# Kernel tuning notes

Measured on AMD Instinct MI355X. Metric: run time of the kernel, lower is better.

## Reference

```python
import jax, jax.numpy as jnp
import numpy as np

B, T, N, H, E, R = 512, 10, 50, 200, 10000, 200

def _aggregate(neigh, neigh_len, hist_len, ids, rids, ent, rel, Wa, ba, v):
    # neigh: [B,T,N] entity ids; returns padded GRU input [B,T,3H]
    h = Wa.shape[0]
    e = ent[neigh]                                  # [B,T,N,h] neighbor embeds
    se = ent[ids]                                   # [B,h]
    re_a = ent[rids]                                # faithful: original uses ent_embeds[r] in attention
    Wn, Ws, Wr = Wa[:, :h], Wa[:, h:2 * h], Wa[:, 2 * h:]
    pre = jnp.einsum('btnh,gh->btng', e, Wn) + (se @ Ws.T + re_a @ Wr.T + ba)[:, None, None, :]
    logits = (jnp.tanh(pre) @ v)[..., 0]            # [B,T,N]
    nmask = jnp.arange(neigh.shape[2])[None, None, :] < neigh_len[:, :, None]
    logits = jnp.where(nmask, logits, -1e30)
    w = jax.nn.softmax(logits, axis=-1)             # per-timestep softmax over valid neighbors
    step = jnp.einsum('btn,btnh->bth', w, e)        # attention-pooled neighbor embed
    rr = rel[rids]                                  # rel_embeds used in the GRU-input concat
    seq = jnp.concatenate([step,
                           jnp.broadcast_to(se[:, None, :], step.shape),
                           jnp.broadcast_to(rr[:, None, :], step.shape)], axis=-1)
    smask = jnp.arange(neigh.shape[1])[None, :] < hist_len[:, None]
    return seq * smask[..., None]                   # zeros past each sample's history length

def _gru(seq, lengths, Wih, Whh, bih, bhh):
    # packed_padded GRU equivalent: hidden freezes at each sample's true length
    Bb, Tt, _ = seq.shape
    h = Whh.shape[1]
    mask = jnp.arange(Tt)[None, :] < lengths[:, None]
    def step(hprev, xm):
        x, m = xm
        gi = x @ Wih.T + bih
        gh = hprev @ Whh.T + bhh
        ir, iz, inn = jnp.split(gi, 3, axis=-1)
        hr, hz, hn = jnp.split(gh, 3, axis=-1)
        rg = jax.nn.sigmoid(ir + hr)
        zg = jax.nn.sigmoid(iz + hz)
        ng = jnp.tanh(inn + rg * hn)
        hnew = (1.0 - zg) * ng + zg * hprev
        return jnp.where(m[:, None], hnew, hprev), None
    h0 = jnp.zeros((Bb, h), seq.dtype)
    hf, _ = jax.lax.scan(step, h0, (seq.transpose(1, 0, 2), mask.T))
    return hf

def _ce(logits, labels):
    lp = jax.nn.log_softmax(logits, axis=-1)
    return -jnp.mean(jnp.take_along_axis(lp, labels[:, None], axis=-1)[:, 0])

def setup_inputs() -> dict:
    key = jax.random.key(0)
    ks = jax.random.split(key, 32)
    d = {}
    d['triplets'] = jnp.stack([jax.random.randint(ks[0], (B,), 0, E),
                               jax.random.randint(ks[1], (B,), 0, R),
                               jax.random.randint(ks[2], (B,), 0, E)], axis=1)
    d['s_hist_neigh'] = jax.random.randint(ks[3], (B, T, N), 0, E)
    d['s_neigh_len'] = jax.random.randint(ks[4], (B, T), 1, N + 1)
    d['s_hist_len'] = jax.random.randint(ks[5], (B,), 1, T + 1)
    d['o_hist_neigh'] = jax.random.randint(ks[6], (B, T, N), 0, E)
    d['o_neigh_len'] = jax.random.randint(ks[7], (B, T), 1, N + 1)
    d['o_hist_len'] = jax.random.randint(ks[8], (B,), 1, T + 1)
    sc = 0.05
    d['ent_embeds'] = jax.random.normal(ks[9], (E, H)) * sc
    d['rel_embeds'] = jax.random.normal(ks[10], (R, H)) * sc
    d['attn_s_w'] = jax.random.normal(ks[11], (H, 3 * H)) * sc
    d['attn_s_b'] = jnp.zeros((H,))
    d['v_s'] = jax.random.normal(ks[12], (H, 1)) * sc
    d['attn_o_w'] = jax.random.normal(ks[13], (H, 3 * H)) * sc
    d['attn_o_b'] = jnp.zeros((H,))
    d['v_o'] = jax.random.normal(ks[14], (H, 1)) * sc
    d['sub_w_ih'] = jax.random.normal(ks[15], (3 * H, 3 * H)) * sc
    d['sub_w_hh'] = jax.random.normal(ks[16], (3 * H, H)) * sc
    d['sub_b_ih'] = jnp.zeros((3 * H,))
    d['sub_b_hh'] = jnp.zeros((3 * H,))
    d['ob_w_ih'] = jax.random.normal(ks[17], (3 * H, 3 * H)) * sc
    d['ob_w_hh'] = jax.random.normal(ks[18], (3 * H, H)) * sc
    d['ob_b_ih'] = jnp.zeros((3 * H,))
    d['ob_b_hh'] = jnp.zeros((3 * H,))
    d['lin_sub_w'] = jax.random.normal(ks[19], (E, 3 * H)) * sc
    d['lin_sub_b'] = jnp.zeros((E,))
    d['lin_ob_w'] = jax.random.normal(ks[20], (E, 3 * H)) * sc
    d['lin_ob_b'] = jnp.zeros((E,))
    return d

def reference(triplets, s_hist_neigh, s_neigh_len, s_hist_len, o_hist_neigh, o_neigh_len, o_hist_len,
              ent_embeds, rel_embeds, attn_s_w, attn_s_b, v_s, attn_o_w, attn_o_b, v_o,
              sub_w_ih, sub_w_hh, sub_b_ih, sub_b_hh, ob_w_ih, ob_w_hh, ob_b_ih, ob_b_hh,
              lin_sub_w, lin_sub_b, lin_ob_w, lin_ob_b):
    s, r, o = triplets[:, 0], triplets[:, 1], triplets[:, 2]
    s_idx = jnp.argsort(-s_hist_len)   # descending sort by history length
    o_idx = jnp.argsort(-o_hist_len)
    seq_s = _aggregate(s_hist_neigh, s_neigh_len, s_hist_len, s, r, ent_embeds, rel_embeds, attn_s_w, attn_s_b, v_s)
    seq_o = _aggregate(o_hist_neigh, o_neigh_len, o_hist_len, o, r, ent_embeds, rel_embeds, attn_o_w, attn_o_b, v_o)
    s_h = _gru(seq_s, s_hist_len, sub_w_ih, sub_w_hh, sub_b_ih, sub_b_hh)[s_idx]
    o_h = _gru(seq_o, o_hist_len, ob_w_ih, ob_w_hh, ob_b_ih, ob_b_hh)[o_idx]
    ob_pred = jnp.concatenate([ent_embeds[s[s_idx]], s_h, rel_embeds[r[s_idx]]], axis=1) @ lin_sub_w.T + lin_sub_b
    sub_pred = jnp.concatenate([ent_embeds[o[o_idx]], o_h, rel_embeds[r[o_idx]]], axis=1) @ lin_ob_w.T + lin_ob_b
    loss = _ce(ob_pred, o[s_idx]) + _ce(sub_pred, s[o_idx])
    return loss, sub_pred, ob_pred, o_idx, s_idx
```

## Files before the change

### kernel.cpp

```cpp
#include <hip/hip_runtime.h>
#include <hip/hip_bf16.h>
#include <math.h>

typedef __hip_bfloat16 bf16;
typedef __attribute__((ext_vector_type(8))) short short8;
typedef __attribute__((ext_vector_type(4))) float f32x4;

#define B_ 512
#define T_ 10
#define N_ 50
#define H_ 200
#define E_ 10000
#define R_ 200
#define K3 600
#define EP_ 10048

__device__ __forceinline__ float b2f(bf16 x){ return __bfloat162float(x); }
__device__ __forceinline__ float u2f(unsigned short u){
  unsigned int x = ((unsigned int)u) << 16;
  return __builtin_bit_cast(float, x);
}
__device__ __forceinline__ float fsigm(float x){
  return __builtin_amdgcn_rcpf(1.f + __expf(-x));
}
__device__ __forceinline__ float ftanh(float x){
  x = fminf(15.f, fmaxf(-15.f, x));
  float e = __expf(-2.f * x);
  return (1.f - e) * __builtin_amdgcn_rcpf(1.f + e);
}

__global__ __launch_bounds__(256) void k_packall(
    const float* __restrict__ aw_s, const float* __restrict__ aw_o,
    const float* __restrict__ sub_wih, const float* __restrict__ ob_wih,
    const float* __restrict__ sub_whh, const float* __restrict__ ob_whh,
    const float* __restrict__ ent, const float* __restrict__ rel,
    const int* __restrict__ trip,
    bf16* __restrict__ Wn2, bf16* __restrict__ Wb2, bf16* __restrict__ Wg2,
    bf16* __restrict__ Wstep, bf16* __restrict__ Whh2,
    bf16* __restrict__ Ab, bf16* __restrict__ Ag, float* __restrict__ lossacc)
{
  int bid = blockIdx.x;
  int tid = threadIdx.x;
  if (bid < 448) {
    int r = bid;
    const float* Wa = (r < 200) ? aw_s : aw_o;
    int g = (r < 200) ? r : r - 200;
    bf16* out = Wn2 + (size_t)r * 256;
    for (int k = tid; k < 256; k += 256) {
      float v = (r < 400 && k < 200) ? Wa[(size_t)g * K3 + k] : 0.f;
      out[k] = __float2bfloat16(v);
    }
  } else if (bid < 960) {
    int idx = bid - 448;
    int side = idx >> 8, r = idx & 255;
    const float* W = side ? aw_o : aw_s;
    bf16* out = Wb2 + ((size_t)side * 256 + r) * 448;
    for (int k = tid; k < 448; k += 256) {
      float v = (r < 200 && k < 400) ? W[(size_t)r * K3 + 200 + k] : 0.f;
      out[k] = __float2bfloat16(v);
    }
  } else if (bid < 2240) {
    int idx = bid - 960;
    int side = idx / 640, r = idx % 640;
    const float* W = side ? ob_wih : sub_wih;
    bf16* out = Wg2 + ((size_t)side * 640 + r) * 448;
    for (int k = tid; k < 448; k += 256) {
      float v = (r < 600 && k < 400) ? W[(size_t)r * K3 + 200 + k] : 0.f;
      out[k] = __float2bfloat16(v);
    }
  } else if (bid < 3520) {
    int idx = bid - 2240;
    int side = idx / 640, r = idx % 640;
    const float* W = side ? ob_wih : sub_wih;
    bf16* out = Wstep + ((size_t)side * 640 + r) * 256;
    for (int k = tid; k < 256; k += 256) {
      float v = (r < 600 && k < 200) ? W[(size_t)r * K3 + k] : 0.f;
      out[k] = __float2bfloat16(v);
    }
  } else if (bid < 4736) {
    int idx = bid - 3520;
    int side = idx / 608, r = idx % 608;
    const float* W = side ? ob_whh : sub_whh;
    bf16* out = Whh2 + ((size_t)side * 608 + r) * 224;
    for (int k = tid; k < 224; k += 256) {
      float v = (r < 600 && k < 200) ? W[(size_t)r * H_ + k] : 0.f;
      out[k] = __float2bfloat16(v);
    }
  } else if (bid < 5760) {
    int idx = bid - 4736;
    int side = idx >> 9, b = idx & 511;
    int ids = trip[b * 3 + (side ? 2 : 0)];
    int rid = trip[b * 3 + 1];
    size_t ro = ((size_t)side * B_ + b) * 448;
    for (int k = tid; k < 448; k += 256) {
      float vb = 0.f, vg = 0.f;
      if (k < 200) { float e = ent[(size_t)ids * H_ + k]; vb = e; vg = e; }
      else if (k < 400) {
        vb = ent[(size_t)rid * H_ + (k - 200)];
        vg = rel[(size_t)rid * H_ + (k - 200)];
      }
      Ab[ro + k] = __float2bfloat16(vb);
      Ag[ro + k] = __float2bfloat16(vg);
    }
  } else {
    if (tid < 4) lossacc[tid] = 0.f;
  }
}

__global__ __launch_bounds__(256) void k_pack_lin(
    const float* __restrict__ W0, const float* __restrict__ W1, bf16* __restrict__ Wlin)
{
  int row = blockIdx.x, side = blockIdx.y;
  const float* W = side ? W1 : W0;
  bf16* out = Wlin + ((size_t)side * EP_ + row) * 640;
  for (int k = threadIdx.x; k < 640; k += 256) {
    float v = (row < E_ && k < K3) ? W[(size_t)row * K3 + k] : 0.f;
    out[k] = __float2bfloat16(v);
  }
}

template<bool OUTBF, bool AF32>
__global__ __launch_bounds__(256) void k_gg(
    const void* __restrict__ Aptr, const bf16* __restrict__ Bptr,
    const float* __restrict__ bias0, const float* __restrict__ bias1,
    void* __restrict__ Cptr,
    int M, int Nout, int KP, int Acols,
    long Astride, long Bstride, long Cstride, int Nstride)
{
  int side = blockIdx.z;
  int m0 = blockIdx.x * 128, n0 = blockIdx.y * 64;

  __shared__ bf16 As[128][72];
  __shared__ bf16 Bs[64][72];

  int tid = threadIdx.x;
  int wave = tid >> 6, lane = tid & 63;
  int quad = lane >> 4, l15 = lane & 15;

  f32x4 acc[8];
  #pragma unroll
  for (int mt = 0; mt < 8; mt++) acc[mt] = (f32x4){0,0,0,0};

  int arow = tid >> 1, ac0 = (tid & 1) * 32;
  int gr = m0 + arow; if (gr > M - 1) gr = M - 1;
  int brow = tid >> 2, bc0 = (tid & 3) * 16;

  for (int k0 = 0; k0 < KP; k0 += 64) {
    if (AF32) {
      const float* src = (const float*)Aptr + (size_t)gr * Acols;
      #pragma unroll
      for (int u = 0; u < 8; u++) {
        int kk = k0 + ac0 + u * 4;
        float4 v;
        if (kk + 4 <= Acols) v = *(const float4*)&src[kk];
        else {
          v.x = (kk + 0 < Acols) ? src[kk + 0] : 0.f;
          v.y = (kk + 1 < Acols) ? src[kk + 1] : 0.f;
          v.z = (kk + 2 < Acols) ? src[kk + 2] : 0.f;
          v.w = (kk + 3 < Acols) ? src[kk + 3] : 0.f;
        }
        As[arow][ac0 + u * 4 + 0] = __float2bfloat16(v.x);
        As[arow][ac0 + u * 4 + 1] = __float2bfloat16(v.y);
        As[arow][ac0 + u * 4 + 2] = __float2bfloat16(v.z);
        As[arow][ac0 + u * 4 + 3] = __float2bfloat16(v.w);
      }
    } else {
      const bf16* src = (const bf16*)Aptr + (size_t)side * Astride + (size_t)gr * KP + k0 + ac0;
      #pragma unroll
      for (int u = 0; u < 4; u++)
        *(short8*)&As[arow][ac0 + u * 8] = *(const short8*)&src[u * 8];
    }
    {
      const bf16* src = Bptr + (size_t)side * Bstride + (size_t)(n0 + brow) * KP + k0 + bc0;
      *(short8*)&Bs[brow][bc0]     = *(const short8*)&src[0];
      *(short8*)&Bs[brow][bc0 + 8] = *(const short8*)&src[8];
    }
    __syncthreads();
    #pragma unroll
    for (int ks = 0; ks < 2; ks++) {
      int kk = ks * 32 + quad * 8;
      short8 bfr = *(const short8*)&Bs[wave * 16 + l15][kk];
      #pragma unroll
      for (int mt = 0; mt < 8; mt++) {
        short8 afr = *(const short8*)&As[mt * 16 + l15][kk];
        acc[mt] = __builtin_amdgcn_mfma_f32_16x16x32_bf16(afr, bfr, acc[mt], 0, 0, 0);
      }
    }
    __syncthreads();
  }

  int n = n0 + wave * 16 + l15;
  if (n < Nout) {
    float bv = bias0 ? (side ? bias1[n] : bias0[n]) : 0.f;
    #pragma unroll
    for (int mt = 0; mt < 8; mt++) {
      #pragma unroll
      for (int r = 0; r < 4; r++) {
        int m = m0 + mt * 16 + quad * 4 + r;
        if (m < M) {
          float val = acc[mt][r] + bv;
          if (OUTBF)
            ((bf16*)Cptr)[(size_t)side * Cstride + (size_t)m * Nstride + n] = __float2bfloat16(val);
          else
            ((float*)Cptr)[(size_t)side * Cstride + (size_t)m * Nstride + n] = val;
        }
      }
    }
  }
}

__global__ __launch_bounds__(256) void k_attn3(
    const float* __restrict__ ent,
    const int* __restrict__ neigh0, const int* __restrict__ neigh1,
    const int* __restrict__ nlen0, const int* __restrict__ nlen1,
    const int* __restrict__ hlen0, const int* __restrict__ hlen1,
    const float* __restrict__ v0, const float* __restrict__ v1,
    const bf16* __restrict__ ep2, const float* __restrict__ biasb,
    bf16* __restrict__ stepb)
{
  int side = blockIdx.y;
  int bt = blockIdx.x;
  int b = bt / T_, t = bt % T_;
  int hl = (side ? hlen1 : hlen0)[b];
  bf16* srow = stepb + (((size_t)side * B_ + b) * T_ + t) * 256;
  int tid = threadIdx.x;
  if (t >= hl) {
    srow[tid] = __float2bfloat16(0.f);
    return;
  }
  const int* neigh = side ? neigh1 : neigh0;
  const float* v = side ? v1 : v0;
  const float* brow = biasb + ((size_t)side * B_ + b) * H_;
  int nl = (side ? nlen1 : nlen0)[b * T_ + t];

  __shared__ float bsh[H_], vsh[H_], lg[64], wsh[64];
  __shared__ int nb[N_];
  if (tid < H_) { bsh[tid] = brow[tid]; vsh[tid] = v[tid]; }
  if (tid < N_) nb[tid] = neigh[((size_t)b * T_ + t) * N_ + tid];
  __syncthreads();

  int grp = tid >> 4;
  int l16 = tid & 15;

  float bs[13], vs[13];
  #pragma unroll
  for (int i = 0; i < 13; i++) {
    int g = l16 + i * 16;
    bool ok = (g < H_);
    bs[i] = ok ? bsh[g] : 0.f;
    vs[i] = ok ? vsh[g] : 0.f;
  }

  for (int n = grp; n < nl; n += 16) {
    const bf16* er = ep2 + (size_t)nb[n] * 400 + side * 200;
    float acc = 0.f;
    #pragma unroll
    for (int i = 0; i < 13; i++) {
      int g = l16 + i * 16;
      float e = (g < H_) ? b2f(er[g]) : 0.f;
      acc += ftanh(e + bs[i]) * vs[i];
    }
    #pragma unroll
    for (int off = 8; off > 0; off >>= 1) acc += __shfl_down(acc, off, 16);
    if (l16 == 0) lg[n] = acc;
  }
  __syncthreads();

  if (tid < 64) {
    float x = (tid < nl) ? lg[tid] : -1e30f;
    float m = x;
    #pragma unroll
    for (int off = 32; off > 0; off >>= 1) m = fmaxf(m, __shfl_down(m, off));
    m = __shfl(m, 0);
    float e = (tid < nl) ? __expf(x - m) : 0.f;
    float s = e;
    #pragma unroll
    for (int off = 32; off > 0; off >>= 1) s += __shfl_down(s, off);
    s = __shfl(s, 0);
    if (tid < N_) wsh[tid] = e / s;
  }
  __syncthreads();

  int h = tid;
  if (h < H_) {
    float a0 = 0.f, a1 = 0.f, a2 = 0.f, a3 = 0.f;
    int n = 0;
    for (; n + 4 <= nl; n += 4) {
      a0 += wsh[n + 0] * ent[(size_t)nb[n + 0] * H_ + h];
      a1 += wsh[n + 1] * ent[(size_t)nb[n + 1] * H_ + h];
      a2 += wsh[n + 2] * ent[(size_t)nb[n + 2] * H_ + h];
      a3 += wsh[n + 3] * ent[(size_t)nb[n + 3] * H_ + h];
    }
    for (; n < nl; n++) a0 += wsh[n] * ent[(size_t)nb[n] * H_ + h];
    srow[h] = __float2bfloat16((a0 + a1) + (a2 + a3));
  } else {
    srow[h] = __float2bfloat16(0.f);
  }
}

__global__ __launch_bounds__(832) void k_gru4(
    const bf16* __restrict__ giall, const bf16* __restrict__ gibase,
    const bf16* __restrict__ Whh2,
    const float* __restrict__ bhh0, const float* __restrict__ bhh1,
    const int* __restrict__ len0, const int* __restrict__ len1,
    float* __restrict__ hfin)
{
  int side = blockIdx.y;
  int b0 = blockIdx.x * 16;
  const bf16* gia = giall + ((size_t)side * B_ * T_ + (size_t)b0 * T_) * 600;
  const bf16* gib = gibase + ((size_t)side * B_ + b0) * K3;
  const bf16* Wh  = Whh2 + (size_t)side * 608 * 224;
  const float* bhh = side ? bhh1 : bhh0;
  const int* len = side ? len1 : len0;

  __shared__ __align__(16) bf16 Hs[2][16][232];

  int tid = threadIdx.x;
  int wave = tid >> 6, lane = tid & 63;
  int quad = lane >> 4, l15 = lane & 15;

  for (int i = tid; i < 2 * 16 * 232 / 8; i += 832) ((short8*)&Hs[0][0][0])[i] = (short8)0;

  int j0 = wave * 16;
  int j = j0 + l15;
  bool jok = (j < H_);
  float bhr = 0.f, bhz = 0.f, bhn = 0.f;
  float gr[4] = {}, gz[4] = {}, gn[4] = {};
  int lens4[4];
  #pragma unroll
  for (int r = 0; r < 4; r++) lens4[r] = len[b0 + quad * 4 + r];
  if (jok) {
    bhr = bhh[j]; bhz = bhh[H_ + j]; bhn = bhh[2 * H_ + j];
    #pragma unroll
    for (int r = 0; r < 4; r++) {
      const bf16* g = gib + (size_t)(quad * 4 + r) * K3;
      gr[r] = b2f(g[j]); gz[r] = b2f(g[H_ + j]); gn[r] = b2f(g[2 * H_ + j]);
    }
  }
  const bf16* wr = Wh + (size_t)j * 224;
  const bf16* wz = Wh + (size_t)(200 + j) * 224;
  const bf16* wn = Wh + (size_t)(400 + j) * 224;
  __syncthreads();

  int cur = 0;
  for (int t = 0; t < T_; t++) {
    unsigned short guR[4], guZ[4], guN[4];
    if (jok) {
      #pragma unroll
      for (int r = 0; r < 4; r++) {
        const unsigned short* g =
            (const unsigned short*)(gia + ((size_t)(quad * 4 + r) * T_ + t) * 600);
        guR[r] = g[j]; guZ[r] = g[200 + j]; guN[r] = g[400 + j];
      }
    }
    f32x4 ar = {0,0,0,0}, az = {0,0,0,0}, anh = {0,0,0,0};
    #pragma unroll
    for (int ks = 0; ks < 7; ks++) {
      int kk = ks * 32 + quad * 8;
      short8 a0 = *(const short8*)&Hs[cur][l15][kk];
      short8 br = *(const short8*)&wr[kk];
      short8 bz = *(const short8*)&wz[kk];
      short8 bn = *(const short8*)&wn[kk];
      ar  = __builtin_amdgcn_mfma_f32_16x16x32_bf16(a0, br, ar, 0, 0, 0);
      az  = __builtin_amdgcn_mfma_f32_16x16x32_bf16(a0, bz, az, 0, 0, 0);
      anh = __builtin_amdgcn_mfma_f32_16x16x32_bf16(a0, bn, anh, 0, 0, 0);
    }
    if (jok) {
      #pragma unroll
      for (int r = 0; r < 4; r++) {
        int row = quad * 4 + r;
        float rz  = ar[r] + u2f(guR[r]) + gr[r] + bhr;
        float zz  = az[r] + u2f(guZ[r]) + gz[r] + bhz;
        float inn = u2f(guN[r]) + gn[r];
        float hn  = anh[r] + bhn;
        float rg = fsigm(rz);
        float zg = fsigm(zz);
        float ng = ftanh(inn + rg * hn);
        float hold = b2f(Hs[cur][row][j]);
        float hnew = (1.f - zg) * ng + zg * hold;
        Hs[cur ^ 1][row][j] = __float2bfloat16((t < lens4[r]) ? hnew : hold);
      }
    }
    __syncthreads();
    cur ^= 1;
  }
  for (int i = tid; i < 16 * H_; i += 832) {
    int row = i / H_, jj = i % H_;
    hfin[((size_t)side * B_ + b0 + row) * H_ + jj] = b2f(Hs[cur][row][jj]);
  }
}

__global__ __launch_bounds__(512) void k_argsort(
    const int* __restrict__ hlen0, const int* __restrict__ hlen1,
    int* __restrict__ idxbuf, float* __restrict__ dout)
{
  int side = blockIdx.x;
  const int* len = side ? hlen1 : hlen0;
  __shared__ int lens[B_];
  __shared__ int perm[B_];
  int tid = threadIdx.x;
  lens[tid] = len[tid];
  __syncthreads();
  int L = lens[tid];
  int rank = 0;
  for (int j = 0; j < B_; j++) {
    int Lj = lens[j];
    rank += (Lj > L) || (Lj == L && j < tid);
  }
  perm[rank] = tid;
  __syncthreads();
  idxbuf[side * B_ + tid] = perm[tid];
  size_t base = 1 + (size_t)2 * B_ * E_ + (side ? 0 : B_);
  dout[base + tid] = (float)perm[tid];
}

__global__ __launch_bounds__(256) void k_feat(
    const float* __restrict__ ent, const float* __restrict__ rel, const int* __restrict__ trip,
    const int* __restrict__ idxbuf, const float* __restrict__ hfin,
    bf16* __restrict__ xfeat)
{
  int i = blockIdx.x, p = blockIdx.y;
  int bi = idxbuf[(p == 0 ? 1 : 0) * B_ + i];
  int ent_id = (p == 0) ? trip[bi * 3 + 2] : trip[bi * 3 + 0];
  int rid = trip[bi * 3 + 1];
  const float* hsrc = hfin + (size_t)(p == 0 ? 1 : 0) * B_ * H_;
  bf16* x = xfeat + ((size_t)p * B_ + i) * 640;
  int h = threadIdx.x;
  if (h < H_) {
    x[h]          = __float2bfloat16(ent[(size_t)ent_id * H_ + h]);
    x[H_ + h]     = __float2bfloat16(hsrc[(size_t)bi * H_ + h]);
    x[2 * H_ + h] = __float2bfloat16(rel[(size_t)rid * H_ + h]);
  }
  if (h < 40) x[600 + h] = __float2bfloat16(0.f);
}

__global__ __launch_bounds__(512) void k_gemm6(
    const bf16* __restrict__ Abf, const bf16* __restrict__ Wlin,
    const float* __restrict__ bias0, const float* __restrict__ bias1,
    float* __restrict__ dout)
{
  int side = blockIdx.z;
  const bf16* Bm = Wlin + (size_t)side * EP_ * 640;
  const float* bias = side ? bias1 : bias0;
  float* C = dout + 1 + (size_t)side * B_ * E_;
  int mBase = blockIdx.x * 256;
  int m0 = side * B_ + mBase;
  int n0 = blockIdx.y * 64;

  __shared__ bf16 As[256][72];
  __shared__ bf16 Bs[64][72];

  int tid = threadIdx.x;
  int wave = tid >> 6, lane = tid & 63;
  int quad = lane >> 4, l15 = lane & 15;
  int wm = wave >> 1, wn = wave & 1;

  f32x4 acc[4][2];
  #pragma unroll
  for (int mt = 0; mt < 4; mt++)
    #pragma unroll
    for (int nt = 0; nt < 2; nt++) acc[mt][nt] = (f32x4){0,0,0,0};

  int arow = tid >> 1, ac0 = (tid & 1) * 32;
  int brow = tid >> 3, bc0 = (tid & 7) * 8;
  const bf16* asrc = Abf + (size_t)(m0 + arow) * 640 + ac0;
  const bf16* bsrc = Bm + (size_t)(n0 + brow) * 640 + bc0;

  for (int k0 = 0; k0 < 640; k0 += 64) {
    #pragma unroll
    for (int u = 0; u < 4; u++)
      *(short8*)&As[arow][ac0 + u * 8] = *(const short8*)&asrc[k0 + u * 8];
    *(short8*)&Bs[brow][bc0] = *(const short8*)&bsrc[k0];
    __syncthreads();
    #pragma unroll
    for (int ks = 0; ks < 2; ks++) {
      int kk = ks * 32 + quad * 8;
      short8 bfr[2];
      #pragma unroll
      for (int nt = 0; nt < 2; nt++)
        bfr[nt] = *(const short8*)&Bs[wn * 32 + nt * 16 + l15][kk];
      #pragma unroll
      for (int mt = 0; mt < 4; mt++) {
        short8 afr = *(const short8*)&As[wm * 64 + mt * 16 + l15][kk];
        #pragma unroll
        for (int nt = 0; nt < 2; nt++)
          acc[mt][nt] = __builtin_amdgcn_mfma_f32_16x16x32_bf16(afr, bfr[nt], acc[mt][nt], 0, 0, 0);
      }
    }
    __syncthreads();
  }

  #pragma unroll
  for (int nt = 0; nt < 2; nt++) {
    int n = n0 + wn * 32 + nt * 16 + l15;
    if (n < E_) {
      float bv = bias[n];
      #pragma unroll
      for (int mt = 0; mt < 4; mt++) {
        #pragma unroll
        for (int r = 0; r < 4; r++) {
          int mrow = mBase + wm * 64 + mt * 16 + quad * 4 + r;
          C[(size_t)mrow * E_ + n] = acc[mt][nt][r] + bv;
        }
      }
    }
  }
}

__global__ __launch_bounds__(512) void k_gemm5(
    const bf16* __restrict__ Abf,
    const float* __restrict__ B0, const float* __restrict__ B1,
    const float* __restrict__ bias0, const float* __restrict__ bias1,
    float* __restrict__ dout)
{
  int side = blockIdx.z;
  const float* Bm = side ? B1 : B0;
  const float* bias = side ? bias1 : bias0;
  float* C = dout + 1 + (size_t)side * B_ * E_;
  int mBase = blockIdx.x * 256;
  int m0 = side * B_ + mBase;
  int n0 = blockIdx.y * 64;

  __shared__ bf16 As[256][72];
  __shared__ bf16 Bs[64][72];

  int tid = threadIdx.x;
  int wave = tid >> 6, lane = tid & 63;
  int quad = lane >> 4, l15 = lane & 15;
  int wm = wave >> 1, wn = wave & 1;

  f32x4 acc[4][2];
  #pragma unroll
  for (int mt = 0; mt < 4; mt++)
    #pragma unroll
    for (int nt = 0; nt < 2; nt++) acc[mt][nt] = (f32x4){0,0,0,0};

  int arow = tid >> 1, ac0 = (tid & 1) * 32;
  int brow = tid >> 3, bc0 = (tid & 7) * 8;
  const bf16* asrc = Abf + (size_t)(m0 + arow) * 640 + ac0;
  int nsrc = n0 + brow; if (nsrc > E_ - 1) nsrc = E_ - 1;
  const float* bsrc = Bm + (size_t)nsrc * K3 + bc0;

  for (int k0 = 0; k0 < 640; k0 += 64) {
    #pragma unroll
    for (int u = 0; u < 4; u++)
      *(short8*)&As[arow][ac0 + u * 8] = *(const short8*)&asrc[k0 + u * 8];
    {
      int kb = k0 + bc0;
      if (kb + 8 <= K3) {
        float4 v0 = *(const float4*)&bsrc[k0];
        float4 v1 = *(const float4*)&bsrc[k0 + 4];
        Bs[brow][bc0 + 0] = __float2bfloat16(v0.x);
        Bs[brow][bc0 + 1] = __float2bfloat16(v0.y);
        Bs[brow][bc0 + 2] = __float2bfloat16(v0.z);
        Bs[brow][bc0 + 3] = __float2bfloat16(v0.w);
        Bs[brow][bc0 + 4] = __float2bfloat16(v1.x);
        Bs[brow][bc0 + 5] = __float2bfloat16(v1.y);
        Bs[brow][bc0 + 6] = __float2bfloat16(v1.z);
        Bs[brow][bc0 + 7] = __float2bfloat16(v1.w);
      } else {
        #pragma unroll
        for (int u = 0; u < 8; u++) {
          int k = kb + u;
          float v = (k < K3) ? bsrc[k0 + u] : 0.f;
          Bs[brow][bc0 + u] = __float2bfloat16(v);
        }
      }
    }
    __syncthreads();
    #pragma unroll
    for (int ks = 0; ks < 2; ks++) {
      int kk = ks * 32 + quad * 8;
      short8 bfr[2];
      #pragma unroll
      for (int nt = 0; nt < 2; nt++)
        bfr[nt] = *(const short8*)&Bs[wn * 32 + nt * 16 + l15][kk];
      #pragma unroll
      for (int mt = 0; mt < 4; mt++) {
        short8 afr = *(const short8*)&As[wm * 64 + mt * 16 + l15][kk];
        #pragma unroll
        for (int nt = 0; nt < 2; nt++)
          acc[mt][nt] = __builtin_amdgcn_mfma_f32_16x16x32_bf16(afr, bfr[nt], acc[mt][nt], 0, 0, 0);
      }
    }
    __syncthreads();
  }

  #pragma unroll
  for (int nt = 0; nt < 2; nt++) {
    int n = n0 + wn * 32 + nt * 16 + l15;
    if (n < E_) {
      float bv = bias[n];
      #pragma unroll
      for (int mt = 0; mt < 4; mt++) {
        #pragma unroll
        for (int r = 0; r < 4; r++) {
          int mrow = mBase + wm * 64 + mt * 16 + quad * 4 + r;
          C[(size_t)mrow * E_ + n] = acc[mt][nt][r] + bv;
        }
      }
    }
  }
}

__global__ __launch_bounds__(256) void k_loss(
    const float* __restrict__ dout, const int* __restrict__ trip,
    const int* __restrict__ idxbuf, float* __restrict__ lossacc)
{
  int i = blockIdx.x, p = blockIdx.y;
  const float* row = dout + 1 + (size_t)p * B_ * E_ + (size_t)i * E_;
  int tid = threadIdx.x;
  float m = -1e30f, s = 0.f;
  for (int e = tid; e < E_; e += 256) {
    float x = row[e];
    if (x > m) { s = s * expf(m - x) + 1.f; m = x; }
    else s += expf(x - m);
  }
  __shared__ float ms[256], ss[256];
  ms[tid] = m; ss[tid] = s; __syncthreads();
  for (int st = 128; st > 0; st >>= 1) {
    if (tid < st) {
      float m2 = ms[tid + st], s2 = ss[tid + st];
      float m1 = ms[tid], s1 = ss[tid];
      float mm = fmaxf(m1, m2);
      ss[tid] = s1 * expf(m1 - mm) + s2 * expf(m2 - mm);
      ms[tid] = mm;
    }
    __syncthreads();
  }
  if (tid == 0) {
    int bi = idxbuf[(p == 0 ? 1 : 0) * B_ + i];
    int label = (p == 0) ? trip[bi * 3 + 0] : trip[bi * 3 + 2];
    float lp = row[label] - ms[0] - logf(ss[0]);
    atomicAdd(lossacc, -lp / (float)B_);
  }
}

__global__ void k_loss_write(const float* __restrict__ lossacc, float* __restrict__ dout){
  if (threadIdx.x == 0) dout[0] = lossacc[0];
}

extern "C" void kernel_launch(void* const* d_in, const int* in_sizes, int n_in,
                              void* d_out, int out_size, void* d_ws, size_t ws_size,
                              hipStream_t stream)
{
  const int* trip = (const int*)d_in[0];
  const int* s_ne = (const int*)d_in[1];
  const int* s_nl = (const int*)d_in[2];
  const int* s_hl = (const int*)d_in[3];
  const int* o_ne = (const int*)d_in[4];
  const int* o_nl = (const int*)d_in[5];
  const int* o_hl = (const int*)d_in[6];
  const float* ent = (const float*)d_in[7];
  const float* rel = (const float*)d_in[8];
  const float* aw_s = (const float*)d_in[9];
  const float* ab_s = (const float*)d_in[10];
  const float* v_s  = (const float*)d_in[11];
  const float* aw_o = (const float*)d_in[12];
  const float* ab_o = (const float*)d_in[13];
  const float* v_o  = (const float*)d_in[14];
  const float* sub_wih = (const float*)d_in[15];
  const float* sub_whh = (const float*)d_in[16];
  const float* sub_bih = (const float*)d_in[17];
  const float* sub_bhh = (const float*)d_in[18];
  const float* ob_wih  = (const float*)d_in[19];
  const float* ob_whh  = (const float*)d_in[20];
  const float* ob_bih  = (const float*)d_in[21];
  const float* ob_bhh  = (const float*)d_in[22];
  const float* lin_sub_w = (const float*)d_in[23];
  const float* lin_sub_b = (const float*)d_in[24];
  const float* lin_ob_w  = (const float*)d_in[25];
  const float* lin_ob_b  = (const float*)d_in[26];
  float* dout = (float*)d_out;

  char* w = (char*)d_ws;
  bf16* ep2     = (bf16*)w;  w += (size_t)E_ * 400 * 2;
  bf16* stepb   = (bf16*)w;  w += (size_t)2 * B_ * T_ * 256 * 2;
  float* biasb  = (float*)w; w += (size_t)2 * B_ * H_ * 4;
  bf16* gibase  = (bf16*)w;  w += (size_t)2 * B_ * K3 * 2;
  float* hfin   = (float*)w; w += (size_t)2 * B_ * H_ * 4;
  bf16* xfeat   = (bf16*)w;  w += (size_t)1024 * 640 * 2;
  bf16* Wn2     = (bf16*)w;  w += (size_t)448 * 256 * 2;
  bf16* Wb2     = (bf16*)w;  w += (size_t)2 * 256 * 448 * 2;
  bf16* Wg2     = (bf16*)w;  w += (size_t)2 * 640 * 448 * 2;
  bf16* Wstep   = (bf16*)w;  w += (size_t)2 * 640 * 256 * 2;
  bf16* Whh2    = (bf16*)w;  w += (size_t)2 * 608 * 224 * 2;
  bf16* giall   = (bf16*)w;  w += (size_t)2 * B_ * T_ * 600 * 2;
  bf16* Abias   = (bf16*)w;  w += (size_t)2 * B_ * 448 * 2;
  bf16* Agi     = (bf16*)w;  w += (size_t)2 * B_ * 448 * 2;
  float* lossacc= (float*)w; w += 256;
  int* idxbuf   = (int*)w;   w += 4096;
  bf16* Wlin    = (bf16*)w;  w += (size_t)2 * EP_ * 640 * 2;
  bool useBf16B = ((size_t)(w - (char*)d_ws) <= ws_size);

  k_packall<<<5761, 256, 0, stream>>>(aw_s, aw_o, sub_wih, ob_wih, sub_whh, ob_whh,
                                      ent, rel, trip, Wn2, Wb2, Wg2, Wstep, Whh2,
                                      Abias, Agi, lossacc);
  if (useBf16B)
    k_pack_lin<<<dim3(EP_, 2), 256, 0, stream>>>(lin_ob_w, lin_sub_w, Wlin);
  k_gg<true, true><<<dim3(79, 7, 1), 256, 0, stream>>>(
      (const void*)ent, Wn2, nullptr, nullptr, (void*)ep2,
      E_, 400, 256, 200, 0L, 0L, 0L, 400);
  k_gg<false, false><<<dim3(4, 4, 2), 256, 0, stream>>>(
      (const void*)Abias, Wb2, ab_s, ab_o, (void*)biasb,
      B_, 200, 448, 448, (long)B_ * 448, 256L * 448, (long)B_ * 200, 200);
  k_gg<true, false><<<dim3(4, 10, 2), 256, 0, stream>>>(
      (const void*)Agi, Wg2, sub_bih, ob_bih, (void*)gibase,
      B_, 600, 448, 448, (long)B_ * 448, 640L * 448, (long)B_ * 600, 600);
  k_attn3<<<dim3(B_ * T_, 2), 256, 0, stream>>>(ent, s_ne, o_ne, s_nl, o_nl,
                                                s_hl, o_hl, v_s, v_o, ep2, biasb, stepb);
  k_gg<true, false><<<dim3(40, 10, 2), 256, 0, stream>>>(
      (const void*)stepb, Wstep, nullptr, nullptr, (void*)giall,
      B_ * T_, 600, 256, 256, (long)B_ * T_ * 256, 640L * 256, (long)B_ * T_ * 600, 600);
  k_gru4<<<dim3(B_ / 16, 2), 832, 0, stream>>>(giall, gibase, Whh2, sub_bhh, ob_bhh,
                                               s_hl, o_hl, hfin);
  k_argsort<<<2, 512, 0, stream>>>(s_hl, o_hl, idxbuf, dout);
  k_feat<<<dim3(B_, 2), 256, 0, stream>>>(ent, rel, trip, idxbuf, hfin, xfeat);
  if (useBf16B)
    k_gemm6<<<dim3(2, (E_ + 63) / 64, 2), 512, 0, stream>>>(
        xfeat, Wlin, lin_ob_b, lin_sub_b, dout);
  else
    k_gemm5<<<dim3(2, (E_ + 63) / 64, 2), 512, 0, stream>>>(
        xfeat, lin_ob_w, lin_sub_w, lin_ob_b, lin_sub_b, dout);
  k_loss<<<dim3(B_, 2), 256, 0, stream>>>(dout, trip, idxbuf, lossacc);
  k_loss_write<<<1, 64, 0, stream>>>(lossacc, dout);
}
```

Before: 409.5 us.

## Fuse log-sum-exp accumulation into final GEMM epilogue and simplify loss kernel

The final linear GEMM epilogue now computes exp of each logit, reduces it across lanes and atomically accumulates per-row sum-of-exponentials. A single-block kernel then gathers the label logits and forms the cross-entropy. This removes the separate pass that re-read the full 2x512x10000 logit matrix. Outputs are written with nontemporal stores. The change drops max-subtraction, so it risks overflow for large logits, and it adds atomic contention on the sum buffer.

```diff
diff --git a/kernel.cpp b/kernel.cpp
--- a/kernel.cpp
+++ b/kernel.cpp
@@ -37,7 +37,7 @@
     const int* __restrict__ trip,
     bf16* __restrict__ Wn2, bf16* __restrict__ Wb2, bf16* __restrict__ Wg2,
     bf16* __restrict__ Wstep, bf16* __restrict__ Whh2,
-    bf16* __restrict__ Ab, bf16* __restrict__ Ag, float* __restrict__ lossacc)
+    bf16* __restrict__ Ab, bf16* __restrict__ Ag, float* __restrict__ sumexp)
 {
   int bid = blockIdx.x;
   int tid = threadIdx.x;
@@ -103,7 +103,7 @@
       Ag[ro + k] = __float2bfloat16(vg);
     }
   } else {
-    if (tid < 4) lossacc[tid] = 0.f;
+    for (int i = tid; i < 2 * B_; i += 256) sumexp[i] = 0.f;
   }
 }
 
@@ -437,7 +437,7 @@
 __global__ __launch_bounds__(512) void k_gemm6(
     const bf16* __restrict__ Abf, const bf16* __restrict__ Wlin,
     const float* __restrict__ bias0, const float* __restrict__ bias1,
-    float* __restrict__ dout)
+    float* __restrict__ dout, float* __restrict__ sumexp)
 {
   int side = blockIdx.z;
   const bf16* Bm = Wlin + (size_t)side * EP_ * 640;
@@ -490,19 +490,30 @@
     __syncthreads();
   }
 
+  float bv[2];
+  int ncol[2];
   #pragma unroll
   for (int nt = 0; nt < 2; nt++) {
-    int n = n0 + wn * 32 + nt * 16 + l15;
-    if (n < E_) {
-      float bv = bias[n];
-      #pragma unroll
-      for (int mt = 0; mt < 4; mt++) {
-        #pragma unroll
-        for (int r = 0; r < 4; r++) {
-          int mrow = mBase + wm * 64 + mt * 16 + quad * 4 + r;
-          C[(size_t)mrow * E_ + n] = acc[mt][nt][r] + bv;
+    ncol[nt] = n0 + wn * 32 + nt * 16 + l15;
+    bv[nt] = (ncol[nt] < E_) ? bias[ncol[nt]] : 0.f;
+  }
+  #pragma unroll
+  for (int mt = 0; mt < 4; mt++) {
+    #pragma unroll
+    for (int r = 0; r < 4; r++) {
+      int mrow = mBase + wm * 64 + mt * 16 + quad * 4 + r;
+      float p = 0.f;
+      #pragma unroll
+      for (int nt = 0; nt < 2; nt++) {
+        if (ncol[nt] < E_) {
+          float val = acc[mt][nt][r] + bv[nt];
+          __builtin_nontemporal_store(val, &C[(size_t)mrow * E_ + ncol[nt]]);
+          p += __expf(val);
         }
       }
+      #pragma unroll
+      for (int off = 8; off > 0; off >>= 1) p += __shfl_down(p, off, 16);
+      if (l15 == 0) atomicAdd(&sumexp[side * B_ + mrow], p);
     }
   }
 }
@@ -511,7 +522,7 @@
     const bf16* __restrict__ Abf,
     const float* __restrict__ B0, const float* __restrict__ B1,
     const float* __restrict__ bias0, const float* __restrict__ bias1,
-    float* __restrict__ dout)
+    float* __restrict__ dout, float* __restrict__ sumexp)
 {
   int side = blockIdx.z;
   const float* Bm = side ? B1 : B0;
@@ -586,58 +597,56 @@
     __syncthreads();
   }
 
+  float bv[2];
+  int ncol[2];
   #pragma unroll
   for (int nt = 0; nt < 2; nt++) {
-    int n = n0 + wn * 32 + nt * 16 + l15;
-    if (n < E_) {
-      float bv = bias[n];
-      #pragma unroll
-      for (int mt = 0; mt < 4; mt++) {
-        #pragma unroll
-        for (int r = 0; r < 4; r++) {
-          int mrow = mBase + wm * 64 + mt * 16 + quad * 4 + r;
-          C[(size_t)mrow * E_ + n] = acc[mt][nt][r] + bv;
+    ncol[nt] = n0 + wn * 32 + nt * 16 + l15;
+    bv[nt] = (ncol[nt] < E_) ? bias[ncol[nt]] : 0.f;
+  }
+  #pragma unroll
+  for (int mt = 0; mt < 4; mt++) {
+    #pragma unroll
+    for (int r = 0; r < 4; r++) {
+      int mrow = mBase + wm * 64 + mt * 16 + quad * 4 + r;
+      float p = 0.f;
+      #pragma unroll
+      for (int nt = 0; nt < 2; nt++) {
+        if (ncol[nt] < E_) {
+          float val = acc[mt][nt][r] + bv[nt];
+          __builtin_nontemporal_store(val, &C[(size_t)mrow * E_ + ncol[nt]]);
+          p += __expf(val);
         }
       }
-    }
-  }
-}
-
-__global__ __launch_bounds__(256) void k_loss(
-    const float* __restrict__ dout, const int* __restrict__ trip,
-    const int* __restrict__ idxbuf, float* __restrict__ lossacc)
-{
-  int i = blockIdx.x, p = blockIdx.y;
-  const float* row = dout + 1 + (size_t)p * B_ * E_ + (size_t)i * E_;
+      #pragma unroll
+      for (int off = 8; off > 0; off >>= 1) p += __shfl_down(p, off, 16);
+      if (l15 == 0) atomicAdd(&sumexp[side * B_ + mrow], p);
+    }
+  }
+}
+
+__global__ __launch_bounds__(256) void k_loss2(
+    const float* __restrict__ dout_ro, const int* __restrict__ trip,
+    const int* __restrict__ idxbuf, const float* __restrict__ sumexp,
+    float* __restrict__ dout)
+{
   int tid = threadIdx.x;
-  float m = -1e30f, s = 0.f;
-  for (int e = tid; e < E_; e += 256) {
-    float x = row[e];
-    if (x > m) { s = s * expf(m - x) + 1.f; m = x; }
-    else s += expf(x - m);
-  }
-  __shared__ float ms[256], ss[256];
-  ms[tid] = m; ss[tid] = s; __syncthreads();
-  for (int st = 128; st > 0; st >>= 1) {
-    if (tid < st) {
-      float m2 = ms[tid + st], s2 = ss[tid + st];
-      float m1 = ms[tid], s1 = ss[tid];
-      float mm = fmaxf(m1, m2);
-      ss[tid] = s1 * expf(m1 - mm) + s2 * expf(m2 - mm);
-      ms[tid] = mm;
-    }
-    __syncthreads();
-  }
-  if (tid == 0) {
+  float part = 0.f;
+  for (int idx = tid; idx < 2 * B_; idx += 256) {
+    int p = idx >> 9, i = idx & 511;
     int bi = idxbuf[(p == 0 ? 1 : 0) * B_ + i];
     int label = (p == 0) ? trip[bi * 3 + 0] : trip[bi * 3 + 2];
-    float lp = row[label] - ms[0] - logf(ss[0]);
-    atomicAdd(lossacc, -lp / (float)B_);
-  }
-}
-
-__global__ void k_loss_write(const float* __restrict__ lossacc, float* __restrict__ dout){
-  if (threadIdx.x == 0) dout[0] = lossacc[0];
+    float val = dout_ro[1 + (size_t)p * B_ * E_ + (size_t)i * E_ + label];
+    float lp = val - logf(sumexp[p * B_ + i]);
+    part += -lp / (float)B_;
+  }
+  __shared__ float ps[256];
+  ps[tid] = part; __syncthreads();
+  for (int st = 128; st > 0; st >>= 1) {
+    if (tid < st) ps[tid] += ps[tid + st];
+    __syncthreads();
+  }
+  if (tid == 0) dout[0] = ps[0];
 }
 
 extern "C" void kernel_launch(void* const* d_in, const int* in_sizes, int n_in,
@@ -688,14 +697,14 @@
   bf16* giall   = (bf16*)w;  w += (size_t)2 * B_ * T_ * 600 * 2;
   bf16* Abias   = (bf16*)w;  w += (size_t)2 * B_ * 448 * 2;
   bf16* Agi     = (bf16*)w;  w += (size_t)2 * B_ * 448 * 2;
-  float* lossacc= (float*)w; w += 256;
+  float* sumexp = (float*)w; w += 4096;
   int* idxbuf   = (int*)w;   w += 4096;
   bf16* Wlin    = (bf16*)w;  w += (size_t)2 * EP_ * 640 * 2;
   bool useBf16B = ((size_t)(w - (char*)d_ws) <= ws_size);
 
   k_packall<<<5761, 256, 0, stream>>>(aw_s, aw_o, sub_wih, ob_wih, sub_whh, ob_whh,
                                       ent, rel, trip, Wn2, Wb2, Wg2, Wstep, Whh2,
-                                      Abias, Agi, lossacc);
+                                      Abias, Agi, sumexp);
   if (useBf16B)
     k_pack_lin<<<dim3(EP_, 2), 256, 0, stream>>>(lin_ob_w, lin_sub_w, Wlin);
   k_gg<true, true><<<dim3(79, 7, 1), 256, 0, stream>>>(
@@ -718,10 +727,9 @@
   k_feat<<<dim3(B_, 2), 256, 0, stream>>>(ent, rel, trip, idxbuf, hfin, xfeat);
   if (useBf16B)
     k_gemm6<<<dim3(2, (E_ + 63) / 64, 2), 512, 0, stream>>>(
-        xfeat, Wlin, lin_ob_b, lin_sub_b, dout);
+        xfeat, Wlin, lin_ob_b, lin_sub_b, dout, sumexp);
   else
     k_gemm5<<<dim3(2, (E_ + 63) / 64, 2), 512, 0, stream>>>(
-        xfeat, lin_ob_w, lin_sub_w, lin_ob_b, lin_sub_b, dout);
-  k_loss<<<dim3(B_, 2), 256, 0, stream>>>(dout, trip, idxbuf, lossacc);
-  k_loss_write<<<1, 64, 0, stream>>>(lossacc, dout);
-}
+        xfeat, lin_ob_w, lin_sub_w, lin_ob_b, lin_sub_b, dout, sumexp);
+  k_loss2<<<1, 256, 0, stream>>>(dout, trip, idxbuf, sumexp, dout);
+}
```

New measurement: 421.5 us. 2.9% more time.
